# Kernel tuning notes

Measured on AMD Instinct MI355X. Metric: run time of the kernel, lower is better.

Reference implementation:

```python
import jax, jax.numpy as jnp
import numpy as np

N_NODES = 100000
N_EDGES = 1600000
D_FEAT = 128


def setup_inputs() -> dict:
    key = jax.random.key(0)
    k1, k2, k3 = jax.random.split(key, 3)
    feat = jax.random.normal(k1, (N_NODES, D_FEAT), dtype=jnp.float32)
    src = jax.random.randint(k2, (N_EDGES,), 0, N_NODES, dtype=jnp.int32)
    dst = jax.random.randint(k3, (N_EDGES,), 0, N_NODES, dtype=jnp.int32)
    return {"feat": feat, "src": src, "dst": dst}


def reference(feat, src, dst):
    n = feat.shape[0]
    ones = jnp.ones(src.shape[0], dtype=feat.dtype)
    # out-degree of each node (as message source), clamped to >= 1
    deg_o = jnp.clip(jax.ops.segment_sum(ones, src, num_segments=n), 1.0)
    norm_l = deg_o ** -0.5  # [N]
    feat_scaled = feat * norm_l[:, None]
    # copy_u + sum aggregation: gather from src, scatter-add to dst
    agg = jax.ops.segment_sum(feat_scaled[src], dst, num_segments=n)
    # in-degree normalization on destination side
    deg_i = jnp.clip(jax.ops.segment_sum(ones, dst, num_segments=n), 1.0)
    norm_r = deg_i ** -0.5
    return agg * norm_r[:, None]
```

## Files before the change

### kernel.cpp

```cpp
#include <hip/hip_runtime.h>
#include <hip/hip_fp16.h>

#define D_FEAT      128
#define SCAN_B      1024
#define S_BIN       256
#define BUCKET_BITS 7
#define BUCKET_SZ   128
#define NB_MAX      1024
#define SORT_CAP    6144

typedef float f32x2 __attribute__((ext_vector_type(2)));

__global__ void binhist2_kernel(const int* __restrict__ src, const int* __restrict__ dst,
                                int* __restrict__ part2, int n_edges, int nb, int N2,
                                int slice_len) {
    __shared__ int hd[NB_MAX];
    __shared__ int hs[NB_MAX];
    int s = blockIdx.x;
    for (int i = threadIdx.x; i < nb; i += blockDim.x) { hd[i] = 0; hs[i] = 0; }
    __syncthreads();
    int beg = s * slice_len;
    int end = beg + slice_len; if (end > n_edges) end = n_edges;
    for (int i = beg + threadIdx.x; i < end; i += blockDim.x) {
        atomicAdd(&hd[dst[i] >> BUCKET_BITS], 1);
        atomicAdd(&hs[src[i] >> BUCKET_BITS], 1);
    }
    __syncthreads();
    for (int b = threadIdx.x; b < nb; b += blockDim.x) {
        part2[(size_t)b * S_BIN + s] = hd[b];
        part2[(size_t)(N2 + b * S_BIN) + s] = hs[b];
    }
}

__global__ __launch_bounds__(SCAN_B) void scan1_kernel(const int* __restrict__ in,
        int* __restrict__ off, int* __restrict__ bsum, int n) {
    __shared__ int sh[SCAN_B];
    int t = threadIdx.x;
    int g = blockIdx.x * SCAN_B + t;
    int v = (g < n) ? in[g] : 0;
    sh[t] = v;
    __syncthreads();
    for (int d = 1; d < SCAN_B; d <<= 1) {
        int x = (t >= d) ? sh[t - d] : 0;
        __syncthreads();
        sh[t] += x;
        __syncthreads();
    }
    if (g < n) off[g] = sh[t] - v;
    if (t == SCAN_B - 1) bsum[blockIdx.x] = sh[t];
}

__global__ __launch_bounds__(SCAN_B) void scan2_kernel(int* __restrict__ bsum, int nb) {
    __shared__ int sh[SCAN_B];
    int t = threadIdx.x;
    int v = (t < nb) ? bsum[t] : 0;
    sh[t] = v;
    __syncthreads();
    for (int d = 1; d < SCAN_B; d <<= 1) {
        int x = (t >= d) ? sh[t - d] : 0;
        __syncthreads();
        sh[t] += x;
        __syncthreads();
    }
    if (t < nb) bsum[t] = sh[t] - v;
}

__global__ void scanadd_kernel(int* __restrict__ data, const int* __restrict__ bsum, int n) {
    int i = blockIdx.x * blockDim.x + threadIdx.x;
    if (i < n) data[i] += bsum[i >> 10];
}

__global__ void binscatter2_kernel(const int* __restrict__ src, const int* __restrict__ dst,
                                   const int* __restrict__ offb, int* __restrict__ colp,
                                   unsigned char* __restrict__ colp_src,
                                   int n_edges, int nb, int N2, int slice_len) {
    __shared__ int cd[NB_MAX];
    __shared__ int cs[NB_MAX];
    int s = blockIdx.x;
    for (int b = threadIdx.x; b < nb; b += blockDim.x) {
        cd[b] = offb[(size_t)b * S_BIN + s];
        cs[b] = offb[(size_t)(N2 + b * S_BIN) + s] - n_edges;
    }
    __syncthreads();
    int beg = s * slice_len;
    int end = beg + slice_len; if (end > n_edges) end = n_edges;
    for (int i = beg + threadIdx.x; i < end; i += blockDim.x) {
        int d = dst[i], sv = src[i];
        int pD = atomicAdd(&cd[d >> BUCKET_BITS], 1);
        colp[pD] = sv | ((d & (BUCKET_SZ - 1)) << 20);
        int pS = atomicAdd(&cs[sv >> BUCKET_BITS], 1);
        colp_src[pS] = (unsigned char)(sv & (BUCKET_SZ - 1));
    }
}

__global__ __launch_bounds__(256) void sortbucket_kernel(
        int* __restrict__ colp, const int* __restrict__ offb,
        int* __restrict__ node_off, int n_nodes, int n_edges, int nb) {
    __shared__ int buf[SORT_CAP];
    __shared__ int cnt[BUCKET_SZ];
    __shared__ int sa[BUCKET_SZ];
    __shared__ int sb[BUCKET_SZ];
    int b = blockIdx.x, tid = threadIdx.x;
    int beg = offb[(size_t)b * S_BIN];
    int end = (b + 1 < nb) ? offb[(size_t)(b + 1) * S_BIN] : n_edges;
    int m = end - beg;
    if (tid < BUCKET_SZ) cnt[tid] = 0;
    __syncthreads();
    for (int i = tid; i < m; i += blockDim.x) {
        int v = colp[beg + i];
        if (i < SORT_CAP) buf[i] = v;
        atomicAdd(&cnt[(v >> 20) & (BUCKET_SZ - 1)], 1);
    }
    __syncthreads();
    int* rp = sa; int* wp = sb;
    if (tid < BUCKET_SZ) sa[tid] = cnt[tid];
    __syncthreads();
    for (int d = 1; d < BUCKET_SZ; d <<= 1) {
        if (tid < BUCKET_SZ) wp[tid] = rp[tid] + (tid >= d ? rp[tid - d] : 0);
        __syncthreads();
        int* t = rp; rp = wp; wp = t;
    }
    int node0 = b << BUCKET_BITS;
    int bn = n_nodes - node0; if (bn > BUCKET_SZ) bn = BUCKET_SZ;
    if (tid < BUCKET_SZ) {
        int ex = rp[tid] - cnt[tid];
        wp[tid] = ex;
        if (tid < bn) node_off[node0 + tid] = beg + ex;
    }
    if (b == nb - 1 && tid == 0) node_off[n_nodes] = end;
    __syncthreads();
    int mm = m < SORT_CAP ? m : SORT_CAP;
    for (int i = tid; i < mm; i += blockDim.x) {
        int v = buf[i];
        int p = atomicAdd(&wp[(v >> 20) & (BUCKET_SZ - 1)], 1);
        colp[beg + p] = v & 0xFFFFF;
    }
}

__global__ void countsrc_kernel(const unsigned char* __restrict__ colp_src,
                                const int* __restrict__ offb, float* __restrict__ norm_l,
                                int n_nodes, int n_edges, int nb, int N2) {
    __shared__ int cnt[BUCKET_SZ];
    int b = blockIdx.x, tid = threadIdx.x;
    int beg = offb[(size_t)(N2 + b * S_BIN)] - n_edges;
    int end = (b + 1 < nb) ? offb[(size_t)(N2 + (b + 1) * S_BIN)] - n_edges : n_edges;
    if (tid < BUCKET_SZ) cnt[tid] = 0;
    __syncthreads();
    for (int i = beg + tid; i < end; i += blockDim.x)
        atomicAdd(&cnt[colp_src[i]], 1);
    __syncthreads();
    int node0 = b << BUCKET_BITS;
    int bn = n_nodes - node0; if (bn > BUCKET_SZ) bn = BUCKET_SZ;
    if (tid < bn) {
        int c = cnt[tid]; if (c < 1) c = 1;
        norm_l[node0 + tid] = rsqrtf((float)c);
    }
}

__global__ void convert_kernel(const float* __restrict__ feat, const float* __restrict__ norm_l,
                               __half* __restrict__ feat16, int n_nodes) {
    int t = blockIdx.x * blockDim.x + threadIdx.x;
    int total = n_nodes * (D_FEAT / 8);
    if (t >= total) return;
    float nl = norm_l[t >> 4];
    const float4* fp = (const float4*)feat + (size_t)t * 2;
    float4 a = fp[0], b = fp[1];
    __half2 h0 = __floats2half2_rn(a.x * nl, a.y * nl);
    __half2 h1 = __floats2half2_rn(a.z * nl, a.w * nl);
    __half2 h2 = __floats2half2_rn(b.x * nl, b.y * nl);
    __half2 h3 = __floats2half2_rn(b.z * nl, b.w * nl);
    uint4 o;
    o.x = *(unsigned int*)&h0; o.y = *(unsigned int*)&h1;
    o.z = *(unsigned int*)&h2; o.w = *(unsigned int*)&h3;
    ((uint4*)feat16)[t] = o;
}

__global__ __launch_bounds__(256) void pull_csr_kernel(
        const __half* __restrict__ feat16, const int* __restrict__ col,
        const int* __restrict__ node_off, float* __restrict__ out, int n_nodes) {
    int wid  = (int)(((long long)blockIdx.x * blockDim.x + threadIdx.x) >> 6);
    int lane = threadIdx.x & 63;
    if (wid >= n_nodes) return;
    int s = __builtin_amdgcn_readfirstlane(node_off[wid]);
    int e = __builtin_amdgcn_readfirstlane(node_off[wid + 1]);
    float accx = 0.f, accy = 0.f;
    const __half2* lrow = (const __half2*)feat16 + lane;

    for (int base = s; base < e; base += 64) {
        int m = e - base; if (m > 64) m = 64;
        int cv = (lane < m) ? col[base + lane] : 0;
        int k = 0;
        for (; k + 8 <= m; k += 8) {
            #pragma unroll
            for (int j = 0; j < 8; ++j) {
                int idx = __shfl(cv, k + j, 64);
                __half2 h = lrow[(size_t)(unsigned)idx << 6];
                float2 f = __half22float2(h);
                accx += f.x; accy += f.y;
            }
        }
        for (; k < m; ++k) {
            int idx = __shfl(cv, k, 64);
            __half2 h = lrow[(size_t)(unsigned)idx << 6];
            float2 f = __half22float2(h);
            accx += f.x; accy += f.y;
        }
    }

    int cnt = e - s; if (cnt < 1) cnt = 1;
    float nr = rsqrtf((float)cnt);
    f32x2 r; r.x = accx * nr; r.y = accy * nr;
    __builtin_nontemporal_store(r, (f32x2*)(out + (size_t)wid * D_FEAT) + lane);
}

extern "C" void kernel_launch(void* const* d_in, const int* in_sizes, int n_in,
                              void* d_out, int out_size, void* d_ws, size_t ws_size,
                              hipStream_t stream) {
    const float* feat = (const float*)d_in[0];
    const int*   src  = (const int*)d_in[1];
    const int*   dst  = (const int*)d_in[2];
    float* out = (float*)d_out;

    const int n_nodes = in_sizes[0] / D_FEAT;
    const int n_edges = in_sizes[1];
    const int nb = (n_nodes + BUCKET_SZ - 1) / BUCKET_SZ;
    const int N2 = nb * S_BIN;
    const int NSCAN = 2 * N2;
    const int sl = (n_edges + S_BIN - 1) / S_BIN;

    auto alignup = [](size_t x) { return (x + 255) & ~(size_t)255; };
    char* p = (char*)d_ws;
    int*    node_off = (int*)p;            p += alignup((size_t)(n_nodes + 1) * 4);
    float*  norm_l   = (float*)p;          p += alignup((size_t)n_nodes * 4);
    int*    part2    = (int*)p;            p += alignup((size_t)NSCAN * 4);
    int*    offb     = (int*)p;            p += alignup((size_t)NSCAN * 4);
    int*    bsum     = (int*)p;            p += alignup((size_t)SCAN_B * 4);
    int*    colp     = (int*)p;            p += alignup((size_t)n_edges * 4);
    unsigned char* colp_src = (unsigned char*)p; p += alignup((size_t)n_edges);
    __half* feat16   = (__half*)p;

    binhist2_kernel<<<S_BIN, 256, 0, stream>>>(src, dst, part2, n_edges, nb, N2, sl);

    {
        int nsb = (NSCAN + SCAN_B - 1) / SCAN_B;
        scan1_kernel<<<nsb, SCAN_B, 0, stream>>>(part2, offb, bsum, NSCAN);
        scan2_kernel<<<1, SCAN_B, 0, stream>>>(bsum, nsb);
        scanadd_kernel<<<(NSCAN + 255) / 256, 256, 0, stream>>>(offb, bsum, NSCAN);
    }

    binscatter2_kernel<<<S_BIN, 256, 0, stream>>>(src, dst, offb, colp, colp_src,
                                                  n_edges, nb, N2, sl);

    sortbucket_kernel<<<nb, 256, 0, stream>>>(colp, offb, node_off, n_nodes, n_edges, nb);

    countsrc_kernel<<<nb, 256, 0, stream>>>(colp_src, offb, norm_l, n_nodes, n_edges, nb, N2);

    {
        int total = n_nodes * (D_FEAT / 8);
        convert_kernel<<<(total + 255) / 256, 256, 0, stream>>>(feat, norm_l, feat16, n_nodes);
    }

    {
        long long total = (long long)n_nodes * 64;
        pull_csr_kernel<<<(int)((total + 255) / 256), 256, 0, stream>>>(feat16, colp, node_off,
                                                                        out, n_nodes);
    }
}
```

Measured before the change: 239.1 us.

## Fuse scan-add and count kernels, restructure pull kernel with 16B gathers

Drops the scanadd kernel by having consumers add the block prefix on the fly, and merges sortbucket and countsrc into one launch split by block index. The pull kernel now handles two nodes per wavefront, with 16 lanes each loading a 16-byte fp16 row chunk across two edges in parallel, followed by a shuffle reduction. The binning slice count is doubled and the convert kernel uses nontemporal loads. The new pull layout trades wider loads and fewer wavefronts for some lane divergence when the two paired nodes have unequal degrees.

```diff
diff --git a/kernel.cpp b/kernel.cpp
--- a/kernel.cpp
+++ b/kernel.cpp
@@ -3,13 +3,13 @@
 
 #define D_FEAT      128
 #define SCAN_B      1024
-#define S_BIN       256
+#define S_BIN       512
 #define BUCKET_BITS 7
 #define BUCKET_SZ   128
 #define NB_MAX      1024
 #define SORT_CAP    6144
 
-typedef float f32x2 __attribute__((ext_vector_type(2)));
+typedef float f32x4 __attribute__((ext_vector_type(4)));
 
 __global__ void binhist2_kernel(const int* __restrict__ src, const int* __restrict__ dst,
                                 int* __restrict__ part2, int n_edges, int nb, int N2,
@@ -32,12 +32,12 @@
     }
 }
 
-__global__ __launch_bounds__(SCAN_B) void scan1_kernel(const int* __restrict__ in,
-        int* __restrict__ off, int* __restrict__ bsum, int n) {
+__global__ __launch_bounds__(SCAN_B) void scan1_kernel(int* __restrict__ data,
+        int* __restrict__ bsum, int n) {
     __shared__ int sh[SCAN_B];
     int t = threadIdx.x;
     int g = blockIdx.x * SCAN_B + t;
-    int v = (g < n) ? in[g] : 0;
+    int v = (g < n) ? data[g] : 0;
     sh[t] = v;
     __syncthreads();
     for (int d = 1; d < SCAN_B; d <<= 1) {
@@ -46,7 +46,7 @@
         sh[t] += x;
         __syncthreads();
     }
-    if (g < n) off[g] = sh[t] - v;
+    if (g < n) data[g] = sh[t] - v;
     if (t == SCAN_B - 1) bsum[blockIdx.x] = sh[t];
 }
 
@@ -65,21 +65,18 @@
     if (t < nb) bsum[t] = sh[t] - v;
 }
 
-__global__ void scanadd_kernel(int* __restrict__ data, const int* __restrict__ bsum, int n) {
-    int i = blockIdx.x * blockDim.x + threadIdx.x;
-    if (i < n) data[i] += bsum[i >> 10];
-}
-
 __global__ void binscatter2_kernel(const int* __restrict__ src, const int* __restrict__ dst,
-                                   const int* __restrict__ offb, int* __restrict__ colp,
-                                   unsigned char* __restrict__ colp_src,
+                                   const int* __restrict__ loff, const int* __restrict__ bsum,
+                                   int* __restrict__ colp, unsigned char* __restrict__ colp_src,
                                    int n_edges, int nb, int N2, int slice_len) {
     __shared__ int cd[NB_MAX];
     __shared__ int cs[NB_MAX];
     int s = blockIdx.x;
     for (int b = threadIdx.x; b < nb; b += blockDim.x) {
-        cd[b] = offb[(size_t)b * S_BIN + s];
-        cs[b] = offb[(size_t)(N2 + b * S_BIN) + s] - n_edges;
+        size_t iD = (size_t)b * S_BIN + s;
+        size_t iS = (size_t)N2 + (size_t)b * S_BIN + s;
+        cd[b] = loff[iD] + bsum[iD >> 10];
+        cs[b] = loff[iS] + bsum[iS >> 10] - n_edges;
     }
     __syncthreads();
     int beg = s * slice_len;
@@ -93,16 +90,48 @@
     }
 }
 
-__global__ __launch_bounds__(256) void sortbucket_kernel(
-        int* __restrict__ colp, const int* __restrict__ offb,
-        int* __restrict__ node_off, int n_nodes, int n_edges, int nb) {
+__global__ __launch_bounds__(256) void sortcount_kernel(
+        int* __restrict__ colp, const unsigned char* __restrict__ colp_src,
+        const int* __restrict__ loff, const int* __restrict__ bsum,
+        int* __restrict__ node_off, float* __restrict__ norm_l,
+        int n_nodes, int n_edges, int nb, int N2) {
     __shared__ int buf[SORT_CAP];
     __shared__ int cnt[BUCKET_SZ];
     __shared__ int sa[BUCKET_SZ];
     __shared__ int sb[BUCKET_SZ];
-    int b = blockIdx.x, tid = threadIdx.x;
-    int beg = offb[(size_t)b * S_BIN];
-    int end = (b + 1 < nb) ? offb[(size_t)(b + 1) * S_BIN] : n_edges;
+    int tid = threadIdx.x;
+
+    if ((int)blockIdx.x >= nb) {
+        int b = blockIdx.x - nb;
+        size_t iA = (size_t)N2 + (size_t)b * S_BIN;
+        int beg = loff[iA] + bsum[iA >> 10] - n_edges;
+        int end;
+        if (b + 1 < nb) {
+            size_t iB = (size_t)N2 + (size_t)(b + 1) * S_BIN;
+            end = loff[iB] + bsum[iB >> 10] - n_edges;
+        } else end = n_edges;
+        if (tid < BUCKET_SZ) cnt[tid] = 0;
+        __syncthreads();
+        for (int i = beg + tid; i < end; i += blockDim.x)
+            atomicAdd(&cnt[colp_src[i]], 1);
+        __syncthreads();
+        int node0 = b << BUCKET_BITS;
+        int bn = n_nodes - node0; if (bn > BUCKET_SZ) bn = BUCKET_SZ;
+        if (tid < bn) {
+            int c = cnt[tid]; if (c < 1) c = 1;
+            norm_l[node0 + tid] = rsqrtf((float)c);
+        }
+        return;
+    }
+
+    int b = blockIdx.x;
+    size_t iA = (size_t)b * S_BIN;
+    int beg = loff[iA] + bsum[iA >> 10];
+    int end;
+    if (b + 1 < nb) {
+        size_t iB = (size_t)(b + 1) * S_BIN;
+        end = loff[iB] + bsum[iB >> 10];
+    } else end = n_edges;
     int m = end - beg;
     if (tid < BUCKET_SZ) cnt[tid] = 0;
     __syncthreads();
@@ -137,34 +166,15 @@
     }
 }
 
-__global__ void countsrc_kernel(const unsigned char* __restrict__ colp_src,
-                                const int* __restrict__ offb, float* __restrict__ norm_l,
-                                int n_nodes, int n_edges, int nb, int N2) {
-    __shared__ int cnt[BUCKET_SZ];
-    int b = blockIdx.x, tid = threadIdx.x;
-    int beg = offb[(size_t)(N2 + b * S_BIN)] - n_edges;
-    int end = (b + 1 < nb) ? offb[(size_t)(N2 + (b + 1) * S_BIN)] - n_edges : n_edges;
-    if (tid < BUCKET_SZ) cnt[tid] = 0;
-    __syncthreads();
-    for (int i = beg + tid; i < end; i += blockDim.x)
-        atomicAdd(&cnt[colp_src[i]], 1);
-    __syncthreads();
-    int node0 = b << BUCKET_BITS;
-    int bn = n_nodes - node0; if (bn > BUCKET_SZ) bn = BUCKET_SZ;
-    if (tid < bn) {
-        int c = cnt[tid]; if (c < 1) c = 1;
-        norm_l[node0 + tid] = rsqrtf((float)c);
-    }
-}
-
 __global__ void convert_kernel(const float* __restrict__ feat, const float* __restrict__ norm_l,
                                __half* __restrict__ feat16, int n_nodes) {
     int t = blockIdx.x * blockDim.x + threadIdx.x;
     int total = n_nodes * (D_FEAT / 8);
     if (t >= total) return;
     float nl = norm_l[t >> 4];
-    const float4* fp = (const float4*)feat + (size_t)t * 2;
-    float4 a = fp[0], b = fp[1];
+    const f32x4* fp = (const f32x4*)feat + (size_t)t * 2;
+    f32x4 a = __builtin_nontemporal_load(fp);
+    f32x4 b = __builtin_nontemporal_load(fp + 1);
     __half2 h0 = __floats2half2_rn(a.x * nl, a.y * nl);
     __half2 h1 = __floats2half2_rn(a.z * nl, a.w * nl);
     __half2 h2 = __floats2half2_rn(b.x * nl, b.y * nl);
@@ -178,39 +188,58 @@
 __global__ __launch_bounds__(256) void pull_csr_kernel(
         const __half* __restrict__ feat16, const int* __restrict__ col,
         const int* __restrict__ node_off, float* __restrict__ out, int n_nodes) {
+    int lane = threadIdx.x & 63;
     int wid  = (int)(((long long)blockIdx.x * blockDim.x + threadIdx.x) >> 6);
-    int lane = threadIdx.x & 63;
-    if (wid >= n_nodes) return;
-    int s = __builtin_amdgcn_readfirstlane(node_off[wid]);
-    int e = __builtin_amdgcn_readfirstlane(node_off[wid + 1]);
-    float accx = 0.f, accy = 0.f;
-    const __half2* lrow = (const __half2*)feat16 + lane;
-
-    for (int base = s; base < e; base += 64) {
-        int m = e - base; if (m > 64) m = 64;
-        int cv = (lane < m) ? col[base + lane] : 0;
-        int k = 0;
-        for (; k + 8 <= m; k += 8) {
-            #pragma unroll
-            for (int j = 0; j < 8; ++j) {
-                int idx = __shfl(cv, k + j, 64);
-                __half2 h = lrow[(size_t)(unsigned)idx << 6];
-                float2 f = __half22float2(h);
-                accx += f.x; accy += f.y;
+    int h  = lane >> 5;
+    int g  = (lane >> 4) & 1;
+    int dl = lane & 15;
+    int node = wid * 2 + h;
+    bool nvalid = node < n_nodes;
+    int nsafe = nvalid ? node : n_nodes - 1;
+    int s = node_off[nsafe];
+    int e = nvalid ? node_off[nsafe + 1] : s;
+    int m = e - s;
+    int om = __shfl_xor(m, 32, 64);
+    int mm = m > om ? m : om;
+
+    float a0=0.f,a1=0.f,a2=0.f,a3=0.f,a4=0.f,a5=0.f,a6=0.f,a7=0.f;
+    const uint4* rowb = (const uint4*)feat16;
+
+    for (int base = 0; base < mm; base += 32) {
+        int remh = m - base;
+        int cl = lane & 31;
+        int ci = cl;
+        if (ci >= remh) ci = (remh > 0) ? remh - 1 : 0;
+        int cv = col[s + base + ci];
+        int lim = mm - base; if (lim > 32) lim = 32;
+        for (int k = 0; k < lim; k += 2) {
+            int srcl = (lane & 32) + k + g;
+            int idx = __shfl(cv, srcl, 64);
+            if (base + k + g < m) {
+                uint4 hv = rowb[((size_t)(unsigned)idx << 4) + dl];
+                float2 f;
+                f = __half22float2(*(__half2*)&hv.x); a0 += f.x; a1 += f.y;
+                f = __half22float2(*(__half2*)&hv.y); a2 += f.x; a3 += f.y;
+                f = __half22float2(*(__half2*)&hv.z); a4 += f.x; a5 += f.y;
+                f = __half22float2(*(__half2*)&hv.w); a6 += f.x; a7 += f.y;
             }
         }
-        for (; k < m; ++k) {
-            int idx = __shfl(cv, k, 64);
-            __half2 h = lrow[(size_t)(unsigned)idx << 6];
-            float2 f = __half22float2(h);
-            accx += f.x; accy += f.y;
-        }
-    }
-
-    int cnt = e - s; if (cnt < 1) cnt = 1;
-    float nr = rsqrtf((float)cnt);
-    f32x2 r; r.x = accx * nr; r.y = accy * nr;
-    __builtin_nontemporal_store(r, (f32x2*)(out + (size_t)wid * D_FEAT) + lane);
+    }
+
+    a0 += __shfl_xor(a0, 16, 64); a1 += __shfl_xor(a1, 16, 64);
+    a2 += __shfl_xor(a2, 16, 64); a3 += __shfl_xor(a3, 16, 64);
+    a4 += __shfl_xor(a4, 16, 64); a5 += __shfl_xor(a5, 16, 64);
+    a6 += __shfl_xor(a6, 16, 64); a7 += __shfl_xor(a7, 16, 64);
+
+    if (nvalid && g == 0) {
+        int c = m < 1 ? 1 : m;
+        float nr = rsqrtf((float)c);
+        f32x4 o0 = {a0 * nr, a1 * nr, a2 * nr, a3 * nr};
+        f32x4 o1 = {a4 * nr, a5 * nr, a6 * nr, a7 * nr};
+        f32x4* op = (f32x4*)(out + (size_t)node * D_FEAT) + dl * 2;
+        __builtin_nontemporal_store(o0, op);
+        __builtin_nontemporal_store(o1, op + 1);
+    }
 }
 
 extern "C" void kernel_launch(void* const* d_in, const int* in_sizes, int n_in,
@@ -233,7 +262,6 @@
     int*    node_off = (int*)p;            p += alignup((size_t)(n_nodes + 1) * 4);
     float*  norm_l   = (float*)p;          p += alignup((size_t)n_nodes * 4);
     int*    part2    = (int*)p;            p += alignup((size_t)NSCAN * 4);
-    int*    offb     = (int*)p;            p += alignup((size_t)NSCAN * 4);
     int*    bsum     = (int*)p;            p += alignup((size_t)SCAN_B * 4);
     int*    colp     = (int*)p;            p += alignup((size_t)n_edges * 4);
     unsigned char* colp_src = (unsigned char*)p; p += alignup((size_t)n_edges);
@@ -243,17 +271,15 @@
 
     {
         int nsb = (NSCAN + SCAN_B - 1) / SCAN_B;
-        scan1_kernel<<<nsb, SCAN_B, 0, stream>>>(part2, offb, bsum, NSCAN);
+        scan1_kernel<<<nsb, SCAN_B, 0, stream>>>(part2, bsum, NSCAN);
         scan2_kernel<<<1, SCAN_B, 0, stream>>>(bsum, nsb);
-        scanadd_kernel<<<(NSCAN + 255) / 256, 256, 0, stream>>>(offb, bsum, NSCAN);
-    }
-
-    binscatter2_kernel<<<S_BIN, 256, 0, stream>>>(src, dst, offb, colp, colp_src,
+    }
+
+    binscatter2_kernel<<<S_BIN, 256, 0, stream>>>(src, dst, part2, bsum, colp, colp_src,
                                                   n_edges, nb, N2, sl);
 
-    sortbucket_kernel<<<nb, 256, 0, stream>>>(colp, offb, node_off, n_nodes, n_edges, nb);
-
-    countsrc_kernel<<<nb, 256, 0, stream>>>(colp_src, offb, norm_l, n_nodes, n_edges, nb, N2);
+    sortcount_kernel<<<2 * nb, 256, 0, stream>>>(colp, colp_src, part2, bsum, node_off,
+                                                 norm_l, n_nodes, n_edges, nb, N2);
 
     {
         int total = n_nodes * (D_FEAT / 8);
@@ -261,7 +287,8 @@
     }
 
     {
-        long long total = (long long)n_nodes * 64;
+        long long waves = ((long long)n_nodes + 1) / 2;
+        long long total = waves * 64;
         pull_csr_kernel<<<(int)((total + 255) / 256), 256, 0, stream>>>(feat16, colp, node_off,
                                                                         out, n_nodes);
     }
```

After: 248.7 us. 1.04x slower.
